# Performance work log

Measured on AMD Instinct MI355X. Metric: run time of the kernel, lower is better.

Reference implementation:

```python
import jax, jax.numpy as jnp
import numpy as np

T, B, D, H = 1024, 64, 512, 512
LN_EPS = 1e-5


def setup_inputs() -> dict:
    key = jax.random.key(0)
    ks = jax.random.split(key, 12)
    s = 1.0 / np.sqrt(D + H)
    def lin(k1, k2):
        W = jax.random.uniform(k1, (D + H, H), jnp.float32, -s, s)
        b = jax.random.uniform(k2, (H,), jnp.float32, -s, s)
        return W, b
    Wf, bf = lin(ks[0], ks[1])
    Wi, bi = lin(ks[2], ks[3])
    Wg, bg = lin(ks[4], ks[5])
    Wo, bo = lin(ks[6], ks[7])
    return {
        "inputs": jax.random.normal(ks[8], (T, B, D), jnp.float32),
        "ln_g": jnp.ones((D + H,), jnp.float32),
        "ln_b": jnp.zeros((D + H,), jnp.float32),
        "Wf": Wf, "bf": bf, "Wi": Wi, "bi": bi,
        "Wg": Wg, "bg": bg, "Wo": Wo, "bo": bo,
    }


def reference(inputs, ln_g, ln_b, Wf, bf, Wi, bi, Wg, bg, Wo, bo):
    # inputs: [T, B, D] time-major, as in the torch module (unbind dim=0)
    Bsz = inputs.shape[1]
    Hd = Wf.shape[1]
    # stack gate weights once: [D+H, 4H] -> single GEMM per step (same math)
    Wall = jnp.concatenate([Wf, Wi, Wg, Wo], axis=1)
    ball = jnp.concatenate([bf, bi, bg, bo], axis=0)

    def step(carry, x):
        hx, cx = carry
        comb = jnp.concatenate([x, hx], axis=1)        # [B, D+H]
        mu = jnp.mean(comb, axis=-1, keepdims=True)
        var = jnp.var(comb, axis=-1, keepdims=True)
        comb = (comb - mu) * jax.lax.rsqrt(var + LN_EPS) * ln_g + ln_b
        z = comb @ Wall + ball                          # [B, 4H]
        f = jax.nn.sigmoid(z[:, 0 * Hd:1 * Hd])
        i = jax.nn.sigmoid(z[:, 1 * Hd:2 * Hd])
        g = jnp.tanh(z[:, 2 * Hd:3 * Hd])
        o = jax.nn.sigmoid(z[:, 3 * Hd:4 * Hd])
        cx = f * cx + i * g
        hx = o * jnp.tanh(cx) + x                       # residual add
        return (hx, cx), hx

    h0 = jnp.zeros((Bsz, Hd), inputs.dtype)
    c0 = jnp.zeros((Bsz, Hd), inputs.dtype)
    (hx, cx), stacked = jax.lax.scan(step, (h0, c0), inputs)
    return stacked, hx, cx
```

## Files before the change

kernel.cpp:

```cpp
#include <hip/hip_runtime.h>
#include <hip/hip_bf16.h>

#define T_STEPS 1024
#define NWG     64

typedef __attribute__((ext_vector_type(8))) short          bf16x8;
typedef __attribute__((ext_vector_type(4))) float          f32x4;
typedef __attribute__((ext_vector_type(8))) unsigned short u16x8;
typedef unsigned long long ull;

static __device__ __forceinline__ unsigned short f2bf_bits(float f) {
    union { __hip_bfloat16 h; unsigned short u; } cv;
    cv.h = __float2bfloat16(f);
    return cv.u;
}

__global__ __launch_bounds__(256) void pack_weights(
    const float* __restrict__ Wf, const float* __restrict__ Wi,
    const float* __restrict__ Wg, const float* __restrict__ Wo,
    const float* __restrict__ ln_g, __hip_bfloat16* __restrict__ pack)
{
    __shared__ unsigned short tile[512 * 32];
    const int blk = blockIdx.x;
    const int g = blk >> 1, part = blk & 1;
    const int tid = threadIdx.x;

    for (int idx = tid; idx < 512 * 32; idx += 256) {
        int kl = idx >> 5, c = idx & 31;
        int q = c >> 3, jl = c & 7;
        int k = part * 512 + kl;
        const float* W = (q == 0) ? Wf : ((q == 1) ? Wi : ((q == 2) ? Wg : Wo));
        float v = W[k * 512 + g * 8 + jl] * ln_g[k];
        tile[kl * 32 + c] = f2bf_bits(v);
    }
    __syncthreads();

    unsigned short* out = (unsigned short*)(pack + (size_t)blk * 16384);
    for (int s = tid; s < 2048; s += 256) {
        int tn = s >> 10, ks = (s >> 6) & 15, l = s & 63;
        u16x8 v;
#pragma unroll
        for (int e = 0; e < 8; ++e) {
            int klocal = ks * 32 + ((l >> 4) * 8) + e;
            int c = tn * 16 + (l & 15);
            v[e] = tile[klocal * 32 + c];
        }
        *(u16x8*)(out + (size_t)s * 8) = v;
    }
}

__global__ __launch_bounds__(256) void compute_sc(
    const float* __restrict__ Wf, const float* __restrict__ Wi,
    const float* __restrict__ Wg, const float* __restrict__ Wo,
    const float* __restrict__ bf_, const float* __restrict__ bi_,
    const float* __restrict__ bg_, const float* __restrict__ bo_,
    const float* __restrict__ ln_g, const float* __restrict__ ln_b,
    float* __restrict__ S, float* __restrict__ C)
{
    int n = blockIdx.x * 256 + threadIdx.x;
    int q = n >> 9, j = n & 511;
    const float* W = (q == 0) ? Wf : ((q == 1) ? Wi : ((q == 2) ? Wg : Wo));
    const float* bb = (q == 0) ? bf_ : ((q == 1) ? bi_ : ((q == 2) ? bg_ : bo_));
    float accS = 0.f, accC = 0.f;
    for (int k = 0; k < 1024; ++k) {
        float w = W[k * 512 + j];
        accS += ln_g[k] * w;
        accC += ln_b[k] * w;
    }
    S[n] = accS;
    C[n] = accC + bb[j];
}

__global__ __launch_bounds__(256) void prep_x(
    const float* __restrict__ x, __hip_bfloat16* __restrict__ xb,
    float* __restrict__ sx, float* __restrict__ sq)
{
    const int wave = threadIdx.x >> 6, lane = threadIdx.x & 63;
    const long row = (long)blockIdx.x * 4 + wave;
    const float* src = x + row * 512 + lane * 8;
    float4 a = *(const float4*)src;
    float4 b = *(const float4*)(src + 4);
    float vals[8] = {a.x, a.y, a.z, a.w, b.x, b.y, b.z, b.w};
    u16x8 o;
    float s = 0.f, qq = 0.f;
#pragma unroll
    for (int e = 0; e < 8; ++e) {
        s += vals[e];
        qq += vals[e] * vals[e];
        o[e] = f2bf_bits(vals[e]);
    }
    *(u16x8*)((unsigned short*)xb + row * 512 + lane * 8) = o;
#pragma unroll
    for (int d = 1; d < 64; d <<= 1) {
        s  += __shfl_xor(s, d);
        qq += __shfl_xor(qq, d);
    }
    if (lane == 0) { sx[row] = s; sq[row] = qq; }
}

__global__ __launch_bounds__(512, 2) void qlstm_main(
    const float* __restrict__ x,
    const __hip_bfloat16* __restrict__ pack,
    const float* __restrict__ Sarr, const float* __restrict__ Carr,
    const __hip_bfloat16* __restrict__ xb,
    const float* __restrict__ sx, const float* __restrict__ sq,
    unsigned short* __restrict__ hxb,
    unsigned int* __restrict__ flags,
    float* __restrict__ out)
{
    const int g = blockIdx.x;
    const int tid = threadIdx.x;
    const int wave = tid >> 6, lane = tid & 63;
    const int m = wave >> 1, kh = wave & 1;
    const int b = tid >> 3, jl = tid & 7, jg = g * 8 + jl;

    __shared__ float zXs[2][2][2112];
    __shared__ float zHs[2][2][2112];
    __shared__ float rsS[2][64][2], rsQ[2][64][2];
    __shared__ float Scol[32], Ccol[32];

    if (tid < 32) {
        int n = (tid >> 3) * 512 + g * 8 + (tid & 7);
        Scol[tid] = Sarr[n];
        Ccol[tid] = Carr[n];
    }

    bf16x8 Bx0[8], Bx1[8], Bh0[8], Bh1[8];
    {
        const bf16x8* px = (const bf16x8*)(pack + (size_t)(g * 2 + 0) * 16384);
        const bf16x8* ph = (const bf16x8*)(pack + (size_t)(g * 2 + 1) * 16384);
#pragma unroll
        for (int i = 0; i < 8; ++i) {
            int ksp = kh * 8 + i;
            Bx0[i] = px[ksp * 64 + lane];
            Bx1[i] = px[1024 + ksp * 64 + lane];
            Bh0[i] = ph[ksp * 64 + lane];
            Bh1[i] = ph[1024 + ksp * 64 + lane];
        }
    }

    const int arow = m * 16 + (lane & 15);
    const int acol = (lane >> 4) * 8;
    const int r0 = m * 16 + (lane >> 4) * 4, c0 = lane & 15;
    float cx = 0.f;

    auto xgemm_store = [&](const bf16x8* af, int par) {
        f32x4 a0 = {0.f, 0.f, 0.f, 0.f}, a1 = {0.f, 0.f, 0.f, 0.f};
#pragma unroll
        for (int ks = 0; ks < 8; ++ks) {
            a0 = __builtin_amdgcn_mfma_f32_16x16x32_bf16(af[ks], Bx0[ks], a0, 0, 0, 0);
            a1 = __builtin_amdgcn_mfma_f32_16x16x32_bf16(af[ks], Bx1[ks], a1, 0, 0, 0);
        }
        float* zb = &zXs[par][kh][0];
#pragma unroll
        for (int r = 0; r < 4; ++r) {
            zb[(r0 + r) * 33 + c0]      = a0[r];
            zb[(r0 + r) * 33 + 16 + c0] = a1[r];
        }
    };

    {
        const bf16x8* Ap = (const bf16x8*)(xb + (size_t)arow * 512 + kh * 256 + acol);
        bf16x8 af[8];
#pragma unroll
        for (int ks = 0; ks < 8; ++ks) af[ks] = Ap[ks * 4];
        xgemm_store(af, 0);
    }

    for (int t = 0; t < T_STEPS; ++t) {
        const int p = t & 1;

        float xres = x[(size_t)t * 32768 + b * 512 + jg];
        float sxv = sx[t * 64 + b];
        float sqv = sq[t * 64 + b];
        bf16x8 afrN[8];
        if (t + 1 < T_STEPS) {
            const bf16x8* Ap = (const bf16x8*)(xb + (size_t)(t + 1) * 32768
                                               + arow * 512 + kh * 256 + acol);
#pragma unroll
            for (int ks = 0; ks < 8; ++ks) afrN[ks] = Ap[ks * 4];
        }

        if (t) {
            const ull* fp_ = (const ull*)(flags + (kh * 32 + (lane & 31)) * 16 + m * 2);
            int slp = 0;
            for (;;) {
                ull v = __hip_atomic_load(fp_, __ATOMIC_RELAXED,
                                          __HIP_MEMORY_SCOPE_AGENT);
                unsigned fa = (unsigned)v, fb = (unsigned)(v >> 32);
                unsigned mn = fa < fb ? fa : fb;
                if (__all((int)mn >= t)) break;
                if      (slp == 0) __builtin_amdgcn_s_sleep(1);
                else if (slp == 1) __builtin_amdgcn_s_sleep(2);
                else if (slp == 2) __builtin_amdgcn_s_sleep(4);
                else               __builtin_amdgcn_s_sleep(8);
                if (slp < 3) ++slp;
            }
            asm volatile("" ::: "memory");
        }

        ull hlo[8], hhi[8];
        {
            const ull* hp = (const ull*)hxb + (size_t)p * 8192;
            const int g0 = kh * 32 + (lane >> 4);
            const int rb = arow * 2;
#pragma unroll
            for (int ks = 0; ks < 8; ++ks) {
                const int idx = (g0 + ks * 4) * 128 + rb;
                hlo[ks] = __hip_atomic_load(hp + idx, __ATOMIC_RELAXED,
                                            __HIP_MEMORY_SCOPE_AGENT);
                hhi[ks] = __hip_atomic_load(hp + idx + 1, __ATOMIC_RELAXED,
                                            __HIP_MEMORY_SCOPE_AGENT);
            }
        }

        {
            f32x4 h0 = {0.f, 0.f, 0.f, 0.f}, h1 = {0.f, 0.f, 0.f, 0.f};
#pragma unroll
            for (int ks = 0; ks < 8; ++ks) {
                union { ull u[2]; bf16x8 v; } cv;
                cv.u[0] = hlo[ks]; cv.u[1] = hhi[ks];
                h0 = __builtin_amdgcn_mfma_f32_16x16x32_bf16(cv.v, Bh0[ks], h0, 0, 0, 0);
                h1 = __builtin_amdgcn_mfma_f32_16x16x32_bf16(cv.v, Bh1[ks], h1, 0, 0, 0);
            }
            float* zb = &zHs[p][kh][0];
#pragma unroll
            for (int r = 0; r < 4; ++r) {
                zb[(r0 + r) * 33 + c0]      = h0[r];
                zb[(r0 + r) * 33 + 16 + c0] = h1[r];
            }
        }

        {
            float s = 0.f, q = 0.f;
#pragma unroll
            for (int ks = 0; ks < 8; ++ks) {
                unsigned uu[4] = { (unsigned)hlo[ks], (unsigned)(hlo[ks] >> 32),
                                   (unsigned)hhi[ks], (unsigned)(hhi[ks] >> 32) };
#pragma unroll
                for (int j = 0; j < 4; ++j) {
                    float f0 = __uint_as_float(uu[j] << 16);
                    float f1 = __uint_as_float(uu[j] & 0xffff0000u);
                    s += f0 + f1;
                    q = fmaf(f0, f0, fmaf(f1, f1, q));
                }
            }
            s += __shfl_xor(s, 16); q += __shfl_xor(q, 16);
            s += __shfl_xor(s, 32); q += __shfl_xor(q, 32);
            if (lane < 16) {
                rsS[p][m * 16 + lane][kh] = s;
                rsQ[p][m * 16 + lane][kh] = q;
            }
        }
        __syncthreads();

        float hval;
        {
            float hs = rsS[p][b][0] + rsS[p][b][1];
            float hq = rsQ[p][b][0] + rsQ[p][b][1];
            float mu = (sxv + hs) * (1.f / 1024.f);
            float var = (sqv + hq) * (1.f / 1024.f) - mu * mu;
            float rs = rsqrtf(var + 1e-5f);

            const float* zx0 = &zXs[p][0][0];
            const float* zx1 = &zXs[p][1][0];
            const float* zh0 = &zHs[p][0][0];
            const float* zh1 = &zHs[p][1][0];
            const int i0 = b * 33;
            float zf = zx0[i0 + jl]      + zx1[i0 + jl]      + zh0[i0 + jl]      + zh1[i0 + jl];
            float zi = zx0[i0 + 8 + jl]  + zx1[i0 + 8 + jl]  + zh0[i0 + 8 + jl]  + zh1[i0 + 8 + jl];
            float zg = zx0[i0 + 16 + jl] + zx1[i0 + 16 + jl] + zh0[i0 + 16 + jl] + zh1[i0 + 16 + jl];
            float zo = zx0[i0 + 24 + jl] + zx1[i0 + 24 + jl] + zh0[i0 + 24 + jl] + zh1[i0 + 24 + jl];
            zf = rs * (zf - mu * Scol[jl])      + Ccol[jl];
            zi = rs * (zi - mu * Scol[8 + jl])  + Ccol[8 + jl];
            zg = rs * (zg - mu * Scol[16 + jl]) + Ccol[16 + jl];
            zo = rs * (zo - mu * Scol[24 + jl]) + Ccol[24 + jl];

            float f  = 1.f / (1.f + __expf(-zf));
            float i_ = 1.f / (1.f + __expf(-zi));
            float gg = 2.f / (1.f + __expf(-2.f * zg)) - 1.f;
            float o_ = 1.f / (1.f + __expf(-zo));
            cx = f * cx + i_ * gg;
            float th = 2.f / (1.f + __expf(-2.f * cx)) - 1.f;
            hval = o_ * th + xres;
        }

        if (t + 1 < T_STEPS) {
            unsigned hb = (unsigned)f2bf_bits(hval);
            unsigned v01 = hb | ((unsigned)__shfl_xor((int)hb, 1) << 16);
            ull v03 = (ull)v01 |
                ((ull)(unsigned)__shfl_xor((int)v01, 2) << 32);
            if ((jl & 3) == 0) {
                ull* hd = (ull*)hxb + (size_t)(p ^ 1) * 8192
                          + g * 128 + b * 2 + (jl >> 2);
                __hip_atomic_store(hd, v03, __ATOMIC_RELAXED,
                                   __HIP_MEMORY_SCOPE_AGENT);
            }
            asm volatile("s_waitcnt vmcnt(0)" ::: "memory");
            if (lane == 0) {
                __hip_atomic_store(flags + g * 16 + wave, (unsigned)(t + 1),
                                   __ATOMIC_RELAXED, __HIP_MEMORY_SCOPE_AGENT);
            }
        }

        out[(size_t)t * 32768 + b * 512 + jg] = hval;
        if (t == T_STEPS - 1) {
            out[(size_t)T_STEPS * 32768 + b * 512 + jg] = hval;
            out[(size_t)T_STEPS * 32768 + 32768 + b * 512 + jg] = cx;
        }

        if (t + 1 < T_STEPS) xgemm_store(afrN, p ^ 1);
    }
}

extern "C" void kernel_launch(void* const* d_in, const int* in_sizes, int n_in,
                              void* d_out, int out_size, void* d_ws, size_t ws_size,
                              hipStream_t stream)
{
    const float* x    = (const float*)d_in[0];
    const float* ln_g = (const float*)d_in[1];
    const float* ln_b = (const float*)d_in[2];
    const float* Wf   = (const float*)d_in[3];
    const float* bf_  = (const float*)d_in[4];
    const float* Wi   = (const float*)d_in[5];
    const float* bi_  = (const float*)d_in[6];
    const float* Wg   = (const float*)d_in[7];
    const float* bg_  = (const float*)d_in[8];
    const float* Wo   = (const float*)d_in[9];
    const float* bo_  = (const float*)d_in[10];

    char* ws = (char*)d_ws;
    size_t off = 0;
    auto take = [&](size_t bytes) -> char* {
        char* p = ws + off;
        off += (bytes + 255) & ~(size_t)255;
        return p;
    };
    __hip_bfloat16* pack = (__hip_bfloat16*)take((size_t)2097152 * 2);
    float* S             = (float*)take(2048 * 4);
    float* C             = (float*)take(2048 * 4);
    __hip_bfloat16* xb   = (__hip_bfloat16*)take((size_t)33554432 * 2);
    float* sx            = (float*)take(65536 * 4);
    float* sq            = (float*)take(65536 * 4);
    char* ctrl = ws + off;
    unsigned short* hxb  = (unsigned short*)take((size_t)2 * 64 * 512 * 2);
    unsigned int* flags  = (unsigned int*)take(64 * 64);
    size_t ctrl_bytes = (size_t)((ws + off) - ctrl);

    hipMemsetAsync(ctrl, 0, ctrl_bytes, stream);
    pack_weights<<<dim3(128), dim3(256), 0, stream>>>(Wf, Wi, Wg, Wo, ln_g, pack);
    compute_sc<<<dim3(8), dim3(256), 0, stream>>>(Wf, Wi, Wg, Wo, bf_, bi_, bg_, bo_,
                                                  ln_g, ln_b, S, C);
    prep_x<<<dim3(16384), dim3(256), 0, stream>>>(x, xb, sx, sq);
    qlstm_main<<<dim3(NWG), dim3(512), 0, stream>>>(x, pack, S, C, xb, sx, sq,
                                                    hxb, flags, (float*)d_out);
}
```

Before: 5.908 ms.

## Replace flag-based step sync with per-element tagged hidden-state words

Removes the separate per-wave flag array and the store-wait-flag sequence. Each hidden value is now written as a 32-bit word holding its bf16 value in the high half and the step number in the low half. Readers spin directly on the hidden-state data until every tag matches the current step. This drops a round trip and the vmcnt drain on the critical recurrence path, at the cost of doubling hidden-state traffic and polling larger loads.

```diff
diff --git a/kernel.cpp b/kernel.cpp
--- a/kernel.cpp
+++ b/kernel.cpp
@@ -104,8 +104,7 @@
     const float* __restrict__ Sarr, const float* __restrict__ Carr,
     const __hip_bfloat16* __restrict__ xb,
     const float* __restrict__ sx, const float* __restrict__ sq,
-    unsigned short* __restrict__ hxb,
-    unsigned int* __restrict__ flags,
+    unsigned int* __restrict__ hxt,
     float* __restrict__ out)
 {
     const int g = blockIdx.x;
@@ -181,69 +180,64 @@
             for (int ks = 0; ks < 8; ++ks) afrN[ks] = Ap[ks * 4];
         }
 
-        if (t) {
-            const ull* fp_ = (const ull*)(flags + (kh * 32 + (lane & 31)) * 16 + m * 2);
+        ull hw[32];
+        {
+            const ull* hp = (const ull*)hxt + (size_t)p * 16384;
+            const int g0 = kh * 32 + (lane >> 4);
+            const int rb = arow * 4;
+            const ull tag2 = ((ull)(unsigned)t << 32) | (unsigned)t;
             int slp = 0;
             for (;;) {
-                ull v = __hip_atomic_load(fp_, __ATOMIC_RELAXED,
-                                          __HIP_MEMORY_SCOPE_AGENT);
-                unsigned fa = (unsigned)v, fb = (unsigned)(v >> 32);
-                unsigned mn = fa < fb ? fa : fb;
-                if (__all((int)mn >= t)) break;
+#pragma unroll
+                for (int ks = 0; ks < 8; ++ks) {
+                    const int idx = (g0 + ks * 4) * 256 + rb;
+#pragma unroll
+                    for (int j = 0; j < 4; ++j)
+                        hw[ks * 4 + j] = __hip_atomic_load(hp + idx + j,
+                            __ATOMIC_RELAXED, __HIP_MEMORY_SCOPE_AGENT);
+                }
+                ull bad = 0;
+#pragma unroll
+                for (int i = 0; i < 32; ++i)
+                    bad |= (hw[i] & 0x0000FFFF0000FFFFull) ^ tag2;
+                if (__all(bad == 0ull)) break;
                 if      (slp == 0) __builtin_amdgcn_s_sleep(1);
                 else if (slp == 1) __builtin_amdgcn_s_sleep(2);
-                else if (slp == 2) __builtin_amdgcn_s_sleep(4);
-                else               __builtin_amdgcn_s_sleep(8);
-                if (slp < 3) ++slp;
+                else               __builtin_amdgcn_s_sleep(4);
+                if (slp < 2) ++slp;
             }
             asm volatile("" ::: "memory");
         }
 
-        ull hlo[8], hhi[8];
-        {
-            const ull* hp = (const ull*)hxb + (size_t)p * 8192;
-            const int g0 = kh * 32 + (lane >> 4);
-            const int rb = arow * 2;
-#pragma unroll
-            for (int ks = 0; ks < 8; ++ks) {
-                const int idx = (g0 + ks * 4) * 128 + rb;
-                hlo[ks] = __hip_atomic_load(hp + idx, __ATOMIC_RELAXED,
-                                            __HIP_MEMORY_SCOPE_AGENT);
-                hhi[ks] = __hip_atomic_load(hp + idx + 1, __ATOMIC_RELAXED,
-                                            __HIP_MEMORY_SCOPE_AGENT);
-            }
-        }
-
         {
             f32x4 h0 = {0.f, 0.f, 0.f, 0.f}, h1 = {0.f, 0.f, 0.f, 0.f};
+            float s = 0.f, q = 0.f;
 #pragma unroll
             for (int ks = 0; ks < 8; ++ks) {
-                union { ull u[2]; bf16x8 v; } cv;
-                cv.u[0] = hlo[ks]; cv.u[1] = hhi[ks];
-                h0 = __builtin_amdgcn_mfma_f32_16x16x32_bf16(cv.v, Bh0[ks], h0, 0, 0, 0);
-                h1 = __builtin_amdgcn_mfma_f32_16x16x32_bf16(cv.v, Bh1[ks], h1, 0, 0, 0);
+                unsigned v[8];
+#pragma unroll
+                for (int j = 0; j < 4; ++j) {
+                    v[2 * j]     = (unsigned)hw[ks * 4 + j];
+                    v[2 * j + 1] = (unsigned)(hw[ks * 4 + j] >> 32);
+                }
+#pragma unroll
+                for (int e = 0; e < 8; ++e) {
+                    float f = __uint_as_float(v[e] & 0xffff0000u);
+                    s += f;
+                    q = fmaf(f, f, q);
+                }
+                union { unsigned u[4]; bf16x8 bv; } fr;
+#pragma unroll
+                for (int j = 0; j < 4; ++j)
+                    fr.u[j] = (v[2 * j] >> 16) | (v[2 * j + 1] & 0xffff0000u);
+                h0 = __builtin_amdgcn_mfma_f32_16x16x32_bf16(fr.bv, Bh0[ks], h0, 0, 0, 0);
+                h1 = __builtin_amdgcn_mfma_f32_16x16x32_bf16(fr.bv, Bh1[ks], h1, 0, 0, 0);
             }
             float* zb = &zHs[p][kh][0];
 #pragma unroll
             for (int r = 0; r < 4; ++r) {
                 zb[(r0 + r) * 33 + c0]      = h0[r];
                 zb[(r0 + r) * 33 + 16 + c0] = h1[r];
-            }
-        }
-
-        {
-            float s = 0.f, q = 0.f;
-#pragma unroll
-            for (int ks = 0; ks < 8; ++ks) {
-                unsigned uu[4] = { (unsigned)hlo[ks], (unsigned)(hlo[ks] >> 32),
-                                   (unsigned)hhi[ks], (unsigned)(hhi[ks] >> 32) };
-#pragma unroll
-                for (int j = 0; j < 4; ++j) {
-                    float f0 = __uint_as_float(uu[j] << 16);
-                    float f1 = __uint_as_float(uu[j] & 0xffff0000u);
-                    s += f0 + f1;
-                    q = fmaf(f0, f0, fmaf(f1, f1, q));
-                }
             }
             s += __shfl_xor(s, 16); q += __shfl_xor(q, 16);
             s += __shfl_xor(s, 32); q += __shfl_xor(q, 32);
@@ -286,21 +280,10 @@
         }
 
         if (t + 1 < T_STEPS) {
-            unsigned hb = (unsigned)f2bf_bits(hval);
-            unsigned v01 = hb | ((unsigned)__shfl_xor((int)hb, 1) << 16);
-            ull v03 = (ull)v01 |
-                ((ull)(unsigned)__shfl_xor((int)v01, 2) << 32);
-            if ((jl & 3) == 0) {
-                ull* hd = (ull*)hxb + (size_t)(p ^ 1) * 8192
-                          + g * 128 + b * 2 + (jl >> 2);
-                __hip_atomic_store(hd, v03, __ATOMIC_RELAXED,
-                                   __HIP_MEMORY_SCOPE_AGENT);
-            }
-            asm volatile("s_waitcnt vmcnt(0)" ::: "memory");
-            if (lane == 0) {
-                __hip_atomic_store(flags + g * 16 + wave, (unsigned)(t + 1),
-                                   __ATOMIC_RELAXED, __HIP_MEMORY_SCOPE_AGENT);
-            }
+            unsigned tagged = ((unsigned)f2bf_bits(hval) << 16)
+                            | (unsigned)(t + 1);
+            __hip_atomic_store(hxt + (size_t)(p ^ 1) * 32768 + g * 512 + b * 8 + jl,
+                               tagged, __ATOMIC_RELAXED, __HIP_MEMORY_SCOPE_AGENT);
         }
 
         out[(size_t)t * 32768 + b * 512 + jg] = hval;
@@ -343,8 +326,7 @@
     float* sx            = (float*)take(65536 * 4);
     float* sq            = (float*)take(65536 * 4);
     char* ctrl = ws + off;
-    unsigned short* hxb  = (unsigned short*)take((size_t)2 * 64 * 512 * 2);
-    unsigned int* flags  = (unsigned int*)take(64 * 64);
+    unsigned int* hxt    = (unsigned int*)take((size_t)2 * 64 * 512 * 4);
     size_t ctrl_bytes = (size_t)((ws + off) - ctrl);
 
     hipMemsetAsync(ctrl, 0, ctrl_bytes, stream);
@@ -353,5 +335,5 @@
                                                   ln_g, ln_b, S, C);
     prep_x<<<dim3(16384), dim3(256), 0, stream>>>(x, xb, sx, sq);
     qlstm_main<<<dim3(NWG), dim3(512), 0, stream>>>(x, pack, S, C, xb, sx, sq,
-                                                    hxb, flags, (float*)d_out);
-}
+                                                    hxt, (float*)d_out);
+}
```

Result: slower. 11.60 ms (+96.4%).
